# Kernel optimization log

Hardware: AMD Instinct MI355X
Metric: run time of the kernel (lower is better)

Reference implementation:

```python
import jax, jax.numpy as jnp
import numpy as np

B, L, V, E, H = 128, 512, 256, 64, 256


def setup_inputs() -> dict:
    key = jax.random.key(0)
    ks = jax.random.split(key, 8)
    x = jax.random.randint(ks[0], (B, L), 0, V, dtype=jnp.int64)
    hidden = jnp.zeros((B, H), dtype=jnp.float32)  # init_hidden path
    emb = jax.random.normal(ks[1], (V, E), dtype=jnp.float32)  # nn.Embedding table
    W_xh = jax.random.normal(ks[2], (E, H), dtype=jnp.float32) * 0.01
    W_hh = jax.random.normal(ks[3], (H, H), dtype=jnp.float32) * 0.01
    b_h = jnp.zeros((H,), dtype=jnp.float32)
    W_hy_w = jax.random.normal(ks[4], (V, H), dtype=jnp.float32) * (1.0 / np.sqrt(H))  # nn.Linear weight
    W_hy_b = jnp.zeros((V,), dtype=jnp.float32)  # nn.Linear bias
    b_y = jnp.zeros((V,), dtype=jnp.float32)     # extra bias added in forward
    return {"x": x, "hidden": hidden, "emb": emb, "W_xh": W_xh, "W_hh": W_hh,
            "b_h": b_h, "W_hy_w": W_hy_w, "W_hy_b": W_hy_b, "b_y": b_y}


def reference(x, hidden, emb, W_xh, W_hh, b_h, W_hy_w, W_hy_b, b_y):
    # x: [B, L] int -> embed: [B, L, E]
    x_embed = emb[x]
    # time-major for the recurrence: [L, B, E]
    x_tm = jnp.transpose(x_embed, (1, 0, 2))

    def step(h_prev, x_t):
        h_t = jnp.tanh(x_t @ W_xh + h_prev @ W_hh + b_h)
        return h_t, h_t

    final_hidden, hs = jax.lax.scan(step, hidden, x_tm)  # hs: [L, B, H]
    output = jnp.transpose(hs, (1, 0, 2))                # [B, L, H]
    # nn.Linear (weight [V,H] + bias) plus extra b_y
    logits = jnp.einsum('blh,vh->blv', output, W_hy_w) + W_hy_b + b_y
    return logits, final_hidden
```

## Files before the change

### kernel.cpp

```cpp
#include <hip/hip_runtime.h>
#include <hip/hip_bf16.h>
#include <stdint.h>

#define B_ 128
#define L_ 512
#define V_ 256
#define E_ 64
#define H_ 256
#define SC 2.885390081777927f

typedef __attribute__((ext_vector_type(8))) __bf16 bf16x8;
typedef __attribute__((ext_vector_type(4))) float f32x4;
typedef __attribute__((ext_vector_type(8))) unsigned short ushort8;

__device__ __forceinline__ unsigned short f2bf(float f) {
    unsigned int u = __builtin_bit_cast(unsigned int, f);
    u += 0x7fffu + ((u >> 16) & 1u);
    return (unsigned short)(u >> 16);
}

__global__ void prologue_kernel(const float* __restrict__ emb,
                                const float* __restrict__ Wxh,
                                const float* __restrict__ bh,
                                const float* __restrict__ Why,
                                const float* __restrict__ Whyb,
                                const float* __restrict__ by,
                                const float* __restrict__ Whh,
                                float* __restrict__ embW2,
                                unsigned short* __restrict__ whyb16,
                                float* __restrict__ bias,
                                unsigned short* __restrict__ whhT16)
{
    int blk = blockIdx.x, tid = threadIdx.x;
    if (blk < V_) {
        float s = bh[tid];
        #pragma unroll 8
        for (int e = 0; e < E_; ++e)
            s = fmaf(emb[blk * E_ + e], Wxh[e * H_ + tid], s);
        embW2[blk * H_ + tid] = s * SC;
    } else if (blk < 2 * V_) {
        int i = (blk - V_) * 256 + tid;
        whyb16[i] = f2bf(Why[i]);
    } else if (blk == 2 * V_) {
        bias[tid] = Whyb[tid] + by[tid];
    } else {
        int c = blk - (2 * V_ + 1);
        whhT16[c * H_ + tid] = f2bf(Whh[tid * H_ + c] * SC);
    }
}

__global__ __launch_bounds__(512, 1) void rnn_rec_kernel(
    const int* __restrict__ x, const float* __restrict__ hidden,
    const float* __restrict__ embW2, const unsigned short* __restrict__ whhT16,
    unsigned short* __restrict__ hs, float* __restrict__ hfin)
{
    __shared__ unsigned short h_lds[2][16 * 256];

    const int tid  = threadIdx.x;
    const int w    = tid >> 6, lane = tid & 63;
    const int l15  = lane & 15, lhi = lane >> 4;
    const int lhi4 = lhi * 4;
    const int b0   = blockIdx.x * 16;
    const int hb0  = w * 32, hb1 = hb0 + 16;
    char* ldsbase  = (char*)&h_lds[0][0];

    const unsigned swzm = (unsigned)((l15 & 7) << 4);
    const unsigned rb2 = (unsigned)(l15 * 512)
                       + ((unsigned)(lhi * 16) ^ (swzm & 0x30u))
                       + (swzm & 0x40u);
    const unsigned wab  = (unsigned)(l15 * 512)
                        + (((unsigned)(hb0 * 2 + lhi * 8)) ^ swzm);
    const unsigned wab1 = wab ^ 32u;

    bf16x8 afrag0[8], afrag1[8];
    #pragma unroll
    for (int kt = 0; kt < 8; ++kt) {
        afrag0[kt] = *(const bf16x8*)(whhT16 + (hb0 + l15) * H_ + kt * 32 + lhi * 8);
        afrag1[kt] = *(const bf16x8*)(whhT16 + (hb1 + l15) * H_ + kt * 32 + lhi * 8);
    }

    for (int i = tid; i < 16 * 256; i += 512) {
        int row = i >> 8, c = i & 255;
        *(unsigned short*)(ldsbase + (row * 512 + ((c * 2) ^ ((row & 7) << 4)))) =
            f2bf(hidden[(b0 + row) * H_ + c]);
    }

    const char* e8 = (const char*)embW2;
    const unsigned go = (unsigned)((hb0 + lhi4) * 4);
    const int* xp = x + (b0 + l15) * L_ + 2;
    char* hsp = (char*)hs + (size_t)(b0 + l15) * L_ * (H_ * 2) + (hb0 + lhi4) * 2;

    int xvA = x[(b0 + l15) * L_ + 0];
    unsigned v0 = ((unsigned)xvA << 10) + go;
    f32x4 eA0 = *(const f32x4*)(e8 + v0);
    f32x4 eA1 = *(const f32x4*)(e8 + v0 + 64);
    int xvB = x[(b0 + l15) * L_ + 1];
    f32x4 eB0, eB1;

    __syncthreads();

    auto phase = [&](f32x4& ec0, f32x4& ec1, f32x4& en0, f32x4& en1,
                     int xg, int& xf, int CB, bool PG, bool PX, bool FIN)
                     __attribute__((always_inline)) {
        if (PG) {
            unsigned vo = ((unsigned)xg << 10) + go;
            en0 = *(const f32x4*)(e8 + vo);
            en1 = *(const f32x4*)(e8 + vo + 64);
        }
        if (PX) { xf = *xp; ++xp; }

        bf16x8 hv[8];
        #pragma unroll
        for (int kt = 0; kt < 8; ++kt)
            hv[kt] = *(const bf16x8*)(ldsbase +
                       (rb2 ^ (unsigned)((kt << 6) | (CB << 13))));
        f32x4 acc0 = ec0, acc1 = ec1;
        #pragma unroll
        for (int kt = 0; kt < 8; ++kt)
            acc0 = __builtin_amdgcn_mfma_f32_16x16x32_bf16(afrag0[kt], hv[kt], acc0, 0, 0, 0);
        #pragma unroll
        for (int kt = 0; kt < 8; ++kt)
            acc1 = __builtin_amdgcn_mfma_f32_16x16x32_bf16(afrag1[kt], hv[kt], acc1, 0, 0, 0);

        f32x4 th0, th1;
        #pragma unroll
        for (int r = 0; r < 4; ++r) {
            float e = __builtin_exp2f(acc0[r]);
            th0[r] = 1.0f - 2.0f * __builtin_amdgcn_rcpf(e + 1.0f);
        }
        uint2 p0, p1;
        asm("v_cvt_pk_bf16_f32 %0, %1, %2" : "=v"(p0.x) : "v"(th0[0]), "v"(th0[1]));
        asm("v_cvt_pk_bf16_f32 %0, %1, %2" : "=v"(p0.y) : "v"(th0[2]), "v"(th0[3]));
        #pragma unroll
        for (int r = 0; r < 4; ++r) {
            float e = __builtin_exp2f(acc1[r]);
            th1[r] = 1.0f - 2.0f * __builtin_amdgcn_rcpf(e + 1.0f);
        }
        asm("v_cvt_pk_bf16_f32 %0, %1, %2" : "=v"(p1.x) : "v"(th1[0]), "v"(th1[1]));
        asm("v_cvt_pk_bf16_f32 %0, %1, %2" : "=v"(p1.y) : "v"(th1[2]), "v"(th1[3]));

        *(uint2*)(ldsbase + (wab  + ((CB ^ 1) << 13))) = p0;
        *(uint2*)(ldsbase + (wab1 + ((CB ^ 1) << 13))) = p1;

        *(uint2*)hsp = p0;
        *(uint2*)(hsp + 32) = p1;
        hsp += 512;

        if (FIN) {
            *(f32x4*)(hfin + (b0 + l15) * H_ + hb0 + lhi4) = th0;
            *(f32x4*)(hfin + (b0 + l15) * H_ + hb1 + lhi4) = th1;
        }

        __builtin_amdgcn_sched_barrier(0);
        asm volatile("s_waitcnt lgkmcnt(0)" ::: "memory");
        __builtin_amdgcn_s_barrier();
        __builtin_amdgcn_sched_barrier(0);
    };

    for (int i = 0; i < 255; ++i) {
        phase(eA0, eA1, eB0, eB1, xvB, xvA, 0, true, true, false);
        phase(eB0, eB1, eA0, eA1, xvA, xvB, 1, true, true, false);
    }
    phase(eA0, eA1, eB0, eB1, xvB, xvA, 0, true, false, false);
    phase(eB0, eB1, eA0, eA1, 0, xvB, 1, false, false, true);
}

__global__ __launch_bounds__(256, 1) void logits_kernel(
    const unsigned short* __restrict__ hs,
    const unsigned short* __restrict__ whyb16,
    const float* __restrict__ bias,
    float* __restrict__ logits)
{
    __shared__ unsigned short a_lds[2][32 * 256];

    const int tid = threadIdx.x;
    const int w = tid >> 6, lane = tid & 63;
    const int l15 = lane & 15, lhi = lane >> 4;
    const size_t rowblk = (size_t)blockIdx.x * 256;

    int col[4];
    #pragma unroll
    for (int n = 0; n < 4; ++n) col[n] = w * 64 + n * 16 + l15;

    bf16x8 bfrag[4][8];
    #pragma unroll
    for (int n = 0; n < 4; ++n)
        #pragma unroll
        for (int kt = 0; kt < 8; ++kt)
            bfrag[n][kt] = *(const bf16x8*)(whyb16 + col[n] * H_ + kt * 32 + lhi * 8);

    float bv[4];
    #pragma unroll
    for (int n = 0; n < 4; ++n) bv[n] = bias[col[n]];

    auto swz = [](unsigned row, unsigned inrow) -> unsigned {
        return row * 512u + (inrow ^ ((row & 7u) << 4));
    };

    #pragma unroll
    for (int ii = 0; ii < 4; ++ii) {
        unsigned Lg = (unsigned)(ii * 256 + tid) * 16u;
        unsigned row = Lg >> 9, inrow = Lg & 511u;
        ushort8 v = *(const ushort8*)((const char*)hs +
                     ((rowblk + row) * 512u + inrow));
        *(ushort8*)((char*)a_lds[0] + swz(row, inrow)) = v;
    }
    __syncthreads();

    for (int c = 0; c < 8; ++c) {
        const int cb = c & 1;
        ushort8 vs[4];
        unsigned srow[4], sinrow[4];
        if (c < 7) {
            #pragma unroll
            for (int ii = 0; ii < 4; ++ii) {
                unsigned Lg = (unsigned)(ii * 256 + tid) * 16u;
                srow[ii] = Lg >> 9; sinrow[ii] = Lg & 511u;
                vs[ii] = *(const ushort8*)((const char*)hs +
                          ((rowblk + (size_t)(c + 1) * 32 + srow[ii]) * 512u + sinrow[ii]));
            }
        }

        #pragma unroll
        for (int m = 0; m < 2; ++m) {
            f32x4 acc[4];
            #pragma unroll
            for (int n = 0; n < 4; ++n) acc[n] = f32x4{0.f, 0.f, 0.f, 0.f};
            #pragma unroll
            for (int kt = 0; kt < 8; ++kt) {
                unsigned rl = (unsigned)(m * 16 + l15);
                bf16x8 a = *(const bf16x8*)((const char*)a_lds[cb] +
                            swz(rl, (unsigned)(kt * 64 + lhi * 16)));
                #pragma unroll
                for (int n = 0; n < 4; ++n)
                    acc[n] = __builtin_amdgcn_mfma_f32_16x16x32_bf16(
                                 a, bfrag[n][kt], acc[n], 0, 0, 0);
            }
            size_t grow = rowblk + (size_t)c * 32 + m * 16 + lhi * 4;
            #pragma unroll
            for (int n = 0; n < 4; ++n)
                #pragma unroll
                for (int r = 0; r < 4; ++r)
                    logits[(grow + r) * V_ + col[n]] = acc[n][r] + bv[n];
        }
        if (c < 7) {
            #pragma unroll
            for (int ii = 0; ii < 4; ++ii)
                *(ushort8*)((char*)a_lds[cb ^ 1] + swz(srow[ii], sinrow[ii])) = vs[ii];
        }
        __syncthreads();
    }
}

extern "C" void kernel_launch(void* const* d_in, const int* in_sizes, int n_in,
                              void* d_out, int out_size, void* d_ws, size_t ws_size,
                              hipStream_t stream) {
    const int*   x      = (const int*)d_in[0];
    const float* hidden = (const float*)d_in[1];
    const float* emb    = (const float*)d_in[2];
    const float* Wxh    = (const float*)d_in[3];
    const float* Whh    = (const float*)d_in[4];
    const float* bh     = (const float*)d_in[5];
    const float* Why    = (const float*)d_in[6];
    const float* Whyb   = (const float*)d_in[7];
    const float* by     = (const float*)d_in[8];

    float* out = (float*)d_out;
    char*  ws  = (char*)d_ws;

    unsigned short* hs     = (unsigned short*)ws;
    float*          embW2  = (float*)(ws + 33554432);
    unsigned short* whyb16 = (unsigned short*)(ws + 33816576);
    float*          bias   = (float*)(ws + 33947648);
    unsigned short* whhT16 = (unsigned short*)(ws + 33948672);

    prologue_kernel<<<2 * V_ + 1 + V_, 256, 0, stream>>>(emb, Wxh, bh, Why, Whyb, by, Whh,
                                                         embW2, whyb16, bias, whhT16);
    rnn_rec_kernel<<<B_ / 16, 512, 0, stream>>>(x, hidden, embW2, whhT16,
                                                hs, out + (size_t)B_ * L_ * V_);
    logits_kernel<<<(B_ * L_) / 256, 256, 0, stream>>>(hs, whyb16, bias, out);
}
```

Before: 485.3 us.

## Halve recurrence block to four waves, each computing four 16-column H tiles

The recurrent kernel now runs 256 threads (4 waves) per block instead of 512. Each wave holds four W_hh fragment sets in registers and computes 64 hidden columns per step instead of 32. The tanh and store work of one tile is interleaved with the MFMAs of the next. This cuts the number of waves taking part in each per-timestep barrier and gives each wave more independent work to hide latency. The cost is twice the serial MFMA work per wave on each step and much higher register pressure, since 32 bf16x8 fragments stay resident.

```diff
diff --git a/kernel.cpp b/kernel.cpp
--- a/kernel.cpp
+++ b/kernel.cpp
@@ -49,7 +49,7 @@
     }
 }
 
-__global__ __launch_bounds__(512, 1) void rnn_rec_kernel(
+__global__ __launch_bounds__(256, 1) void rnn_rec_kernel(
     const int* __restrict__ x, const float* __restrict__ hidden,
     const float* __restrict__ embW2, const unsigned short* __restrict__ whhT16,
     unsigned short* __restrict__ hs, float* __restrict__ hfin)
@@ -61,51 +61,56 @@
     const int l15  = lane & 15, lhi = lane >> 4;
     const int lhi4 = lhi * 4;
     const int b0   = blockIdx.x * 16;
-    const int hb0  = w * 32, hb1 = hb0 + 16;
     char* ldsbase  = (char*)&h_lds[0][0];
 
     const unsigned swzm = (unsigned)((l15 & 7) << 4);
     const unsigned rb2 = (unsigned)(l15 * 512)
                        + ((unsigned)(lhi * 16) ^ (swzm & 0x30u))
                        + (swzm & 0x40u);
-    const unsigned wab  = (unsigned)(l15 * 512)
-                        + (((unsigned)(hb0 * 2 + lhi * 8)) ^ swzm);
-    const unsigned wab1 = wab ^ 32u;
-
-    bf16x8 afrag0[8], afrag1[8];
-    #pragma unroll
-    for (int kt = 0; kt < 8; ++kt) {
-        afrag0[kt] = *(const bf16x8*)(whhT16 + (hb0 + l15) * H_ + kt * 32 + lhi * 8);
-        afrag1[kt] = *(const bf16x8*)(whhT16 + (hb1 + l15) * H_ + kt * 32 + lhi * 8);
-    }
-
-    for (int i = tid; i < 16 * 256; i += 512) {
+    const unsigned wab0 = (unsigned)(l15 * 512)
+                        + (unsigned)(w * 128)
+                        + (((unsigned)(lhi * 8)) ^ (swzm & 0x10u))
+                        + (swzm & 0x60u);
+
+    bf16x8 afrag[4][8];
+    #pragma unroll
+    for (int f = 0; f < 4; ++f)
+        #pragma unroll
+        for (int kt = 0; kt < 8; ++kt)
+            afrag[f][kt] = *(const bf16x8*)(whhT16 +
+                (w * 64 + f * 16 + l15) * H_ + kt * 32 + lhi * 8);
+
+    for (int i = tid; i < 16 * 256; i += 256) {
         int row = i >> 8, c = i & 255;
         *(unsigned short*)(ldsbase + (row * 512 + ((c * 2) ^ ((row & 7) << 4)))) =
             f2bf(hidden[(b0 + row) * H_ + c]);
     }
 
     const char* e8 = (const char*)embW2;
-    const unsigned go = (unsigned)((hb0 + lhi4) * 4);
+    const unsigned go = (unsigned)((w * 64 + lhi4) * 4);
     const int* xp = x + (b0 + l15) * L_ + 2;
-    char* hsp = (char*)hs + (size_t)(b0 + l15) * L_ * (H_ * 2) + (hb0 + lhi4) * 2;
+    char* hsp = (char*)hs + (size_t)(b0 + l15) * L_ * (H_ * 2) + (w * 64 + lhi4) * 2;
 
     int xvA = x[(b0 + l15) * L_ + 0];
-    unsigned v0 = ((unsigned)xvA << 10) + go;
-    f32x4 eA0 = *(const f32x4*)(e8 + v0);
-    f32x4 eA1 = *(const f32x4*)(e8 + v0 + 64);
+    f32x4 eA[4], eB[4];
+    {
+        unsigned v0 = ((unsigned)xvA << 10) + go;
+        #pragma unroll
+        for (int f = 0; f < 4; ++f)
+            eA[f] = *(const f32x4*)(e8 + v0 + f * 64);
+    }
     int xvB = x[(b0 + l15) * L_ + 1];
-    f32x4 eB0, eB1;
 
     __syncthreads();
 
-    auto phase = [&](f32x4& ec0, f32x4& ec1, f32x4& en0, f32x4& en1,
+    auto phase = [&](f32x4 (&ec)[4], f32x4 (&en)[4],
                      int xg, int& xf, int CB, bool PG, bool PX, bool FIN)
                      __attribute__((always_inline)) {
         if (PG) {
             unsigned vo = ((unsigned)xg << 10) + go;
-            en0 = *(const f32x4*)(e8 + vo);
-            en1 = *(const f32x4*)(e8 + vo + 64);
+            #pragma unroll
+            for (int f = 0; f < 4; ++f)
+                en[f] = *(const f32x4*)(e8 + vo + f * 64);
         }
         if (PX) { xf = *xp; ++xp; }
 
@@ -114,41 +119,42 @@
         for (int kt = 0; kt < 8; ++kt)
             hv[kt] = *(const bf16x8*)(ldsbase +
                        (rb2 ^ (unsigned)((kt << 6) | (CB << 13))));
-        f32x4 acc0 = ec0, acc1 = ec1;
-        #pragma unroll
-        for (int kt = 0; kt < 8; ++kt)
-            acc0 = __builtin_amdgcn_mfma_f32_16x16x32_bf16(afrag0[kt], hv[kt], acc0, 0, 0, 0);
-        #pragma unroll
-        for (int kt = 0; kt < 8; ++kt)
-            acc1 = __builtin_amdgcn_mfma_f32_16x16x32_bf16(afrag1[kt], hv[kt], acc1, 0, 0, 0);
-
-        f32x4 th0, th1;
-        #pragma unroll
-        for (int r = 0; r < 4; ++r) {
-            float e = __builtin_exp2f(acc0[r]);
-            th0[r] = 1.0f - 2.0f * __builtin_amdgcn_rcpf(e + 1.0f);
-        }
-        uint2 p0, p1;
-        asm("v_cvt_pk_bf16_f32 %0, %1, %2" : "=v"(p0.x) : "v"(th0[0]), "v"(th0[1]));
-        asm("v_cvt_pk_bf16_f32 %0, %1, %2" : "=v"(p0.y) : "v"(th0[2]), "v"(th0[3]));
-        #pragma unroll
-        for (int r = 0; r < 4; ++r) {
-            float e = __builtin_exp2f(acc1[r]);
-            th1[r] = 1.0f - 2.0f * __builtin_amdgcn_rcpf(e + 1.0f);
-        }
-        asm("v_cvt_pk_bf16_f32 %0, %1, %2" : "=v"(p1.x) : "v"(th1[0]), "v"(th1[1]));
-        asm("v_cvt_pk_bf16_f32 %0, %1, %2" : "=v"(p1.y) : "v"(th1[2]), "v"(th1[3]));
-
-        *(uint2*)(ldsbase + (wab  + ((CB ^ 1) << 13))) = p0;
-        *(uint2*)(ldsbase + (wab1 + ((CB ^ 1) << 13))) = p1;
-
-        *(uint2*)hsp = p0;
-        *(uint2*)(hsp + 32) = p1;
+
+        f32x4 acc[4];
+        #pragma unroll
+        for (int f = 0; f < 4; ++f) acc[f] = ec[f];
+
+        f32x4 th[4];
+        uint2 p[4];
+
+        #pragma unroll
+        for (int kt = 0; kt < 8; ++kt)
+            acc[0] = __builtin_amdgcn_mfma_f32_16x16x32_bf16(afrag[0][kt], hv[kt], acc[0], 0, 0, 0);
+
+        #pragma unroll
+        for (int f = 0; f < 4; ++f) {
+            if (f < 3) {
+                #pragma unroll
+                for (int kt = 0; kt < 8; ++kt)
+                    acc[f + 1] = __builtin_amdgcn_mfma_f32_16x16x32_bf16(
+                                     afrag[f + 1][kt], hv[kt], acc[f + 1], 0, 0, 0);
+            }
+            #pragma unroll
+            for (int r = 0; r < 4; ++r) {
+                float e = __builtin_exp2f(acc[f][r]);
+                th[f][r] = 1.0f - 2.0f * __builtin_amdgcn_rcpf(e + 1.0f);
+            }
+            asm("v_cvt_pk_bf16_f32 %0, %1, %2" : "=v"(p[f].x) : "v"(th[f][0]), "v"(th[f][1]));
+            asm("v_cvt_pk_bf16_f32 %0, %1, %2" : "=v"(p[f].y) : "v"(th[f][2]), "v"(th[f][3]));
+            *(uint2*)(ldsbase + ((wab0 ^ (unsigned)(f << 5)) + ((CB ^ 1) << 13))) = p[f];
+            *(uint2*)(hsp + f * 32) = p[f];
+        }
         hsp += 512;
 
         if (FIN) {
-            *(f32x4*)(hfin + (b0 + l15) * H_ + hb0 + lhi4) = th0;
-            *(f32x4*)(hfin + (b0 + l15) * H_ + hb1 + lhi4) = th1;
+            #pragma unroll
+            for (int f = 0; f < 4; ++f)
+                *(f32x4*)(hfin + (b0 + l15) * H_ + w * 64 + f * 16 + lhi4) = th[f];
         }
 
         __builtin_amdgcn_sched_barrier(0);
@@ -158,11 +164,11 @@
     };
 
     for (int i = 0; i < 255; ++i) {
-        phase(eA0, eA1, eB0, eB1, xvB, xvA, 0, true, true, false);
-        phase(eB0, eB1, eA0, eA1, xvA, xvB, 1, true, true, false);
-    }
-    phase(eA0, eA1, eB0, eB1, xvB, xvA, 0, true, false, false);
-    phase(eB0, eB1, eA0, eA1, 0, xvB, 1, false, false, true);
+        phase(eA, eB, xvB, xvA, 0, true, true, false);
+        phase(eB, eA, xvA, xvB, 1, true, true, false);
+    }
+    phase(eA, eB, xvB, xvA, 0, true, false, false);
+    phase(eB, eA, 0, xvB, 1, false, false, true);
 }
 
 __global__ __launch_bounds__(256, 1) void logits_kernel(
@@ -276,7 +282,7 @@
 
     prologue_kernel<<<2 * V_ + 1 + V_, 256, 0, stream>>>(emb, Wxh, bh, Why, Whyb, by, Whh,
                                                          embW2, whyb16, bias, whhT16);
-    rnn_rec_kernel<<<B_ / 16, 512, 0, stream>>>(x, hidden, embW2, whhT16,
+    rnn_rec_kernel<<<B_ / 16, 256, 0, stream>>>(x, hidden, embW2, whhT16,
                                                 hs, out + (size_t)B_ * L_ * V_);
     logits_kernel<<<(B_ * L_) / 256, 256, 0, stream>>>(hs, whyb16, bias, out);
 }
```

Result: faster. 454.2 us (-6.4%).
